# Performance work log

Measured on AMD Instinct MI355X. Metric: run time of the kernel, lower is better.

Reference implementation:

```python
import jax, jax.numpy as jnp
import numpy as np

EPS = float(np.finfo(np.float32).eps)
SEQ_LEN = 2048
NUM_HEADS = 16
DIM_EMB = 1024
DIM_HEAD = DIM_EMB // NUM_HEADS
DIM_K = DIM_EMB  # module scales by full dim_k, not per-head dim
BATCH = 2


def cosine_positional_encoding(seq_len, dim):
    idx = jnp.arange(seq_len, dtype=jnp.float32)
    scale = 1.0 / (10000.0 ** (jnp.arange(0, dim, 2, dtype=jnp.float32) / dim) + EPS)
    ang = idx[:, None] * scale[None, :]  # [S, dim/2]
    # interleave sin (even) and cos (odd) along last dim -> [S, dim]
    return jnp.stack([jnp.sin(ang), jnp.cos(ang)], axis=-1).reshape(seq_len, dim)


def setup_inputs() -> dict:
    key = jax.random.key(0)
    ks = jax.random.split(key, 5)
    s = DIM_EMB ** -0.5
    return {
        "x": jax.random.normal(ks[0], (BATCH, SEQ_LEN, DIM_EMB), dtype=jnp.float32),
        "Wq": jax.random.normal(ks[1], (DIM_EMB, DIM_EMB), dtype=jnp.float32) * s,
        "Wk": jax.random.normal(ks[2], (DIM_EMB, DIM_EMB), dtype=jnp.float32) * s,
        "Wv": jax.random.normal(ks[3], (DIM_EMB, DIM_EMB), dtype=jnp.float32) * s,
        "Wo": jax.random.normal(ks[4], (DIM_EMB, DIM_EMB), dtype=jnp.float32) * s,
    }


def reference(x, Wq, Wk, Wv, Wo):
    B, S, E = x.shape
    pos = cosine_positional_encoding(S, DIM_HEAD)  # [S, dim_head]
    # projections (bias-free)
    def split_heads(t):
        return t.reshape(B, S, NUM_HEADS, DIM_HEAD).transpose(0, 2, 1, 3)  # [B,H,S,D]
    q = split_heads(x @ Wq) + pos[None, None]
    k = split_heads(x @ Wk) + pos[None, None]
    v = split_heads(x @ Wv)
    scores = jnp.einsum("bhqd,bhkd->bhqk", q, k) * (DIM_K ** -0.5)
    causal_mask = jnp.triu(jnp.ones((S, S), dtype=bool), k=1)
    m_inf = -jnp.finfo(scores.dtype).max
    scores = jnp.where(causal_mask[None, None], m_inf, scores)
    attn = jax.nn.softmax(scores, axis=-1)
    out = jnp.einsum("bhqk,bhkd->bhqd", attn, v)
    out = out.transpose(0, 2, 1, 3).reshape(B, S, E)
    return out @ Wo
```

## Files before the change

kernel.cpp:

```cpp
#include <hip/hip_runtime.h>
#include <math.h>

#define BATCH 2
#define SEQ   2048
#define EMB   1024
#define NHEAD 16
#define DHEAD 64
#define MROWS (BATCH*SEQ)
#define QKS   2048

typedef unsigned int  uint;
typedef unsigned short ushort;
typedef __attribute__((ext_vector_type(8))) short short8;
typedef __attribute__((ext_vector_type(4))) float f32x4;

__device__ __forceinline__ float exp2_fast(float x) {
    return __builtin_amdgcn_exp2f(x);
}

__global__ void pos_init(float* __restrict__ pos) {
    int s = blockIdx.x;
    int d = threadIdx.x;
    int i = d >> 1;
    float expo  = (float)(2 * i) / (float)DHEAD;
    float scale = 1.0f / (powf(10000.0f, expo) + 1.1920928955078125e-07f);
    float ang   = (float)s * scale;
    pos[s * DHEAD + d] = (d & 1) ? cosf(ang) : sinf(ang);
}

__device__ __forceinline__ uint pack_bf16x2(float a, float b) {
    union { float f; uint u; } x, y;
    x.f = a; y.f = b;
    uint ua = x.u + 0x7fffu + ((x.u >> 16) & 1u);
    uint ub = y.u + 0x7fffu + ((y.u >> 16) & 1u);
    return (ua >> 16) | (ub & 0xffff0000u);
}
__device__ __forceinline__ ushort bf16_1(float a) {
    union { float f; uint u; } x; x.f = a;
    return (ushort)((x.u + 0x7fffu + ((x.u >> 16) & 1u)) >> 16);
}
__device__ __forceinline__ uint cvt_pk_bf16(float lo, float hi) {
    uint r;
    asm("v_cvt_pk_bf16_f32 %0, %1, %2" : "=v"(r) : "v"(lo), "v"(hi));
    return r;
}

__device__ __forceinline__ void gll16(const ushort* g, ushort* l) {
    __builtin_amdgcn_global_load_lds(
        (const __attribute__((address_space(1))) uint*)g,
        (__attribute__((address_space(3))) uint*)l, 16, 0, 0);
}

__global__ __launch_bounds__(256) void cvt_bf16(
    const float* __restrict__ in, ushort* __restrict__ out, int n2) {
    int gid = blockIdx.x * 256 + threadIdx.x;
    if (gid < n2) {
        float2 v = ((const float2*)in)[gid];
        ((uint*)out)[gid] = pack_bf16x2(v.x, v.y);
    }
}

__global__ __launch_bounds__(256) void wt_bf16_all(
    const float* __restrict__ Wq, const float* __restrict__ Wk,
    const float* __restrict__ Wv, const float* __restrict__ Wo,
    ushort* __restrict__ Wqkvt, ushort* __restrict__ Wot) {
    __shared__ float tile[32][33];
    const int which = blockIdx.z;
    const float* W = (which == 0) ? Wq : (which == 1) ? Wk : (which == 2) ? Wv : Wo;
    ushort* Wt = (which < 3) ? (Wqkvt + (size_t)which * 1024 * EMB) : Wot;
    const int c0 = blockIdx.x * 32;
    const int r0 = blockIdx.y * 32;
    const int tx = threadIdx.x & 31;
    const int ty = threadIdx.x >> 5;
#pragma unroll
    for (int i = 0; i < 4; ++i)
        tile[ty + i * 8][tx] = W[(size_t)(r0 + ty + i * 8) * EMB + c0 + tx];
    __syncthreads();
#pragma unroll
    for (int i = 0; i < 4; ++i)
        Wt[(size_t)(c0 + ty + i * 8) * EMB + r0 + tx] = bf16_1(tile[tx][ty + i * 8]);
}

#define TK 32
#define SCLQ (0.03125f * 1.44269504088896f)

template<int TMT>
__global__ __launch_bounds__(256) void gemm_mfma_t(
    const ushort* __restrict__ A, const ushort* __restrict__ Bt,
    void* __restrict__ Cv, ushort* __restrict__ VtOut,
    const float* __restrict__ pos, int posmode, int N, int K) {
    constexpr int MI = TMT / 32;
    __shared__ ushort As[TMT * TK];
    __shared__ ushort Bs[128 * TK];

    const int t    = threadIdx.x;
    const int lane = t & 63, w = t >> 6;
    const int quad = lane >> 4, l15 = lane & 15;
    const int bm = blockIdx.x * TMT, bn = blockIdx.y * 128;
    const int wm = (w & 1) * (TMT / 2), wn = (w >> 1) * 64;
    const int r0 = t >> 2, kp = (t & 3) * 8;

    f32x4 acc[MI][4];
#pragma unroll
    for (int mi = 0; mi < MI; ++mi)
#pragma unroll
        for (int ni = 0; ni < 4; ++ni)
            acc[mi][ni] = (f32x4){0.f, 0.f, 0.f, 0.f};

    for (int k0 = 0; k0 < K; k0 += TK) {
        __syncthreads();
#pragma unroll
        for (int i = 0; i < TMT / 64; ++i)
            gll16(A + (size_t)(bm + i * 64 + r0) * K + k0 + kp, &As[i * 2048 + t * 8]);
#pragma unroll
        for (int i = 0; i < 2; ++i)
            gll16(Bt + (size_t)(bn + i * 64 + r0) * K + k0 + kp, &Bs[i * 2048 + t * 8]);
        __syncthreads();

        short8 af[MI], bfv[4];
#pragma unroll
        for (int mi = 0; mi < MI; ++mi)
            af[mi] = *(const short8*)&As[(wm + mi * 16 + l15) * TK + quad * 8];
#pragma unroll
        for (int ni = 0; ni < 4; ++ni)
            bfv[ni] = *(const short8*)&Bs[(wn + ni * 16 + l15) * TK + quad * 8];
#pragma unroll
        for (int mi = 0; mi < MI; ++mi)
#pragma unroll
            for (int ni = 0; ni < 4; ++ni)
                acc[mi][ni] = __builtin_amdgcn_mfma_f32_16x16x32_bf16(
                    af[mi], bfv[ni], acc[mi][ni], 0, 0, 0);
    }

#pragma unroll
    for (int mi = 0; mi < MI; ++mi) {
        const int row0 = bm + wm + mi * 16 + quad * 4;
#pragma unroll
        for (int ni = 0; ni < 4; ++ni) {
            const int col = bn + wn + ni * 16 + l15;
            if (!posmode) {
#pragma unroll
                for (int r = 0; r < 4; ++r)
                    ((float*)Cv)[(size_t)(row0 + r) * N + col] = acc[mi][ni][r];
            } else if (col < 2048) {
#pragma unroll
                for (int r = 0; r < 4; ++r) {
                    const int row = row0 + r;
                    const int s   = row & (SEQ - 1);
                    float v = acc[mi][ni][r] + pos[s * DHEAD + (col & 63)];
                    if (col < 1024) v *= SCLQ;
                    ((ushort*)Cv)[(size_t)row * QKS + col] = bf16_1(v);
                }
            } else {
                const int hh = (col >> 6) & 15;
                const int d  = col & 63;
                const int bb = row0 >> 11;
                const int s0 = row0 & (SEQ - 1);
                uint2 u;
                u.x = pack_bf16x2(acc[mi][ni][0], acc[mi][ni][1]);
                u.y = pack_bf16x2(acc[mi][ni][2], acc[mi][ni][3]);
                *(uint2*)&VtOut[((size_t)(bb * 16 + hh) * 64 + d) * SEQ + s0] = u;
            }
        }
    }
}

#define LDP 72

__global__ __launch_bounds__(256) void attn_mfma8(
    const ushort* __restrict__ QK, const ushort* __restrict__ Vt,
    ushort* __restrict__ AOb) {
    __shared__ ushort Ks[64 * LDP];
    __shared__ ushort Vs[64 * LDP];
    __shared__ ushort Ps[64 * LDP];

    const int bid  = blockIdx.x;
    const int bh   = (bid & 7) + ((bid >> 8) << 3);
    const int qt   = 31 - ((bid >> 3) & 31);
    const int b    = bh >> 4, hd = bh & 15;
    const int t    = threadIdx.x;
    const int lane = t & 63, w = t >> 6;
    const int quad = lane >> 4, l15 = lane & 15;
    const int wrow = w * 16;
    const int sr = t >> 2;
    const int sc = (t & 3) * 16;

    const size_t qkbase = (size_t)b * SEQ * QKS + hd * 64;
    const ushort* kpb = QK + qkbase + 1024 + (size_t)sr * QKS + sc;
    const ushort* vpb = Vt + ((size_t)bh * 64 + sr) * SEQ;

    const ushort* qp = QK + qkbase + (size_t)(qt * 64 + wrow + l15) * QKS + quad * 8;
    const short8 aq0 = *(const short8*)qp;
    const short8 aq1 = *(const short8*)(qp + 32);

    uint4 ka = *(const uint4*)kpb;
    uint4 kb = *(const uint4*)(kpb + 8);
    uint4 va = *(const uint4*)(vpb + sc);
    uint4 vb = *(const uint4*)(vpb + sc + 8);

    f32x4 acc_o[4];
#pragma unroll
    for (int nd = 0; nd < 4; ++nd) acc_o[nd] = (f32x4){0.f, 0.f, 0.f, 0.f};
    float m_l = -3.0e38f, l_l = 0.f;
    const int qrow_g = qt * 64 + wrow + l15;

    for (int kt = 0; kt <= qt; ++kt) {
        __syncthreads();
        *(uint4*)&Ks[sr * LDP + sc]     = ka;
        *(uint4*)&Ks[sr * LDP + sc + 8] = kb;
        *(uint4*)&Vs[sr * LDP + sc]     = va;
        *(uint4*)&Vs[sr * LDP + sc + 8] = vb;
        const int ktn = (kt < qt) ? kt + 1 : qt;
        ka = *(const uint4*)(kpb + (size_t)ktn * 64 * QKS);
        kb = *(const uint4*)(kpb + (size_t)ktn * 64 * QKS + 8);
        va = *(const uint4*)(vpb + ktn * 64 + sc);
        vb = *(const uint4*)(vpb + ktn * 64 + sc + 8);
        __syncthreads();

        float sv[4][4];
        float pmax = -3.0e38f;
        const bool diag = (kt == qt);
        __builtin_amdgcn_s_setprio(1);
#pragma unroll
        for (int kg = 0; kg < 4; ++kg) {
            const short8 ak0 = *(const short8*)&Ks[(kg * 16 + l15) * LDP + quad * 8];
            const short8 ak1 = *(const short8*)&Ks[(kg * 16 + l15) * LDP + 32 + quad * 8];
            f32x4 a = (f32x4){0.f, 0.f, 0.f, 0.f};
            a = __builtin_amdgcn_mfma_f32_16x16x32_bf16(ak0, aq0, a, 0, 0, 0);
            a = __builtin_amdgcn_mfma_f32_16x16x32_bf16(ak1, aq1, a, 0, 0, 0);
            const int keyb = kt * 64 + kg * 16 + quad * 4;
#pragma unroll
            for (int r = 0; r < 4; ++r) {
                float v = a[r];
                if (diag && (keyb + r > qrow_g)) v = -3.0e38f;
                sv[kg][r] = v;
                pmax = fmaxf(pmax, v);
            }
        }
        __builtin_amdgcn_s_setprio(0);
        pmax = fmaxf(pmax, __shfl_xor(pmax, 16, 64));
        pmax = fmaxf(pmax, __shfl_xor(pmax, 32, 64));

        if (__any(pmax - m_l > 8.f)) {
            const float m_new = fmaxf(m_l, pmax);
            const float alpha = exp2_fast(m_l - m_new);
            m_l = m_new;
            l_l *= alpha;
            float av[4];
#pragma unroll
            for (int r = 0; r < 4; ++r) av[r] = __shfl(alpha, quad * 4 + r, 64);
#pragma unroll
            for (int nd = 0; nd < 4; ++nd)
#pragma unroll
                for (int r = 0; r < 4; ++r) acc_o[nd][r] *= av[r];
        }

        float rs = 0.f;
#pragma unroll
        for (int kg = 0; kg < 4; ++kg)
#pragma unroll
            for (int r = 0; r < 4; ++r) {
                float p = exp2_fast(sv[kg][r] - m_l);
                sv[kg][r] = p;
                rs += p;
            }
        rs += __shfl_xor(rs, 16, 64);
        rs += __shfl_xor(rs, 32, 64);
        l_l += rs;

        ushort* Pw = &Ps[wrow * LDP];
#pragma unroll
        for (int kg = 0; kg < 4; ++kg) {
            uint2 u;
            u.x = cvt_pk_bf16(sv[kg][0], sv[kg][1]);
            u.y = cvt_pk_bf16(sv[kg][2], sv[kg][3]);
            *(uint2*)&Pw[l15 * LDP + kg * 16 + quad * 4] = u;
        }
        const short8 pa0 = *(const short8*)&Pw[l15 * LDP + quad * 8];
        const short8 pa1 = *(const short8*)&Pw[l15 * LDP + 32 + quad * 8];
        __builtin_amdgcn_s_setprio(1);
#pragma unroll
        for (int nd = 0; nd < 4; ++nd) {
            const short8 bv0 = *(const short8*)&Vs[(nd * 16 + l15) * LDP + quad * 8];
            const short8 bv1 = *(const short8*)&Vs[(nd * 16 + l15) * LDP + 32 + quad * 8];
            acc_o[nd] = __builtin_amdgcn_mfma_f32_16x16x32_bf16(pa0, bv0, acc_o[nd], 0, 0, 0);
            acc_o[nd] = __builtin_amdgcn_mfma_f32_16x16x32_bf16(pa1, bv1, acc_o[nd], 0, 0, 0);
        }
        __builtin_amdgcn_s_setprio(0);
    }

    float linv[4];
#pragma unroll
    for (int r = 0; r < 4; ++r) linv[r] = 1.0f / __shfl(l_l, quad * 4 + r, 64);
#pragma unroll
    for (int nd = 0; nd < 4; ++nd)
#pragma unroll
        for (int r = 0; r < 4; ++r) {
            const int row = qt * 64 + wrow + quad * 4 + r;
            AOb[(size_t)(b * SEQ + row) * EMB + hd * 64 + nd * 16 + l15] =
                bf16_1(acc_o[nd][r] * linv[r]);
        }
}

#define BM 64
#define BN 64
#define BK 16

__global__ __launch_bounds__(256) void gemm_f32(
    const float* __restrict__ A, const float* __restrict__ B,
    float* __restrict__ C, const float* __restrict__ pos, int addpos,
    int M, int N, int K) {
    __shared__ float As[BK][BM];
    __shared__ float Bs[BK][BN];
    const int tid = threadIdx.x;
    const int bm  = blockIdx.x * BM;
    const int bn  = blockIdx.y * BN;
    const int tx  = tid & 15;
    const int ty  = tid >> 4;
    const int arow = tid >> 2;
    const int acol = (tid & 3) << 2;
    const int brow = tid >> 4;
    const int bcol = (tid & 15) << 2;
    float acc[4][4] = {{0.f}};
    const float* Aptr = A + (size_t)(bm + arow) * K + acol;
    const float* Bptr = B + (size_t)brow * N + bn + bcol;
    for (int k0 = 0; k0 < K; k0 += BK) {
        float4 av = *(const float4*)(Aptr + k0);
        float4 bv = *(const float4*)(Bptr + (size_t)k0 * N);
        __syncthreads();
        As[acol + 0][arow] = av.x;
        As[acol + 1][arow] = av.y;
        As[acol + 2][arow] = av.z;
        As[acol + 3][arow] = av.w;
        *(float4*)&Bs[brow][bcol] = bv;
        __syncthreads();
#pragma unroll
        for (int kk = 0; kk < BK; ++kk) {
            float4 a = *(const float4*)&As[kk][ty << 2];
            float4 b = *(const float4*)&Bs[kk][tx << 2];
            float aa[4] = {a.x, a.y, a.z, a.w};
            float bb[4] = {b.x, b.y, b.z, b.w};
#pragma unroll
            for (int i = 0; i < 4; ++i)
#pragma unroll
                for (int j = 0; j < 4; ++j)
                    acc[i][j] += aa[i] * bb[j];
        }
    }
#pragma unroll
    for (int i = 0; i < 4; ++i) {
        int m = bm + (ty << 2) + i;
        int n = bn + (tx << 2);
        float4 v = make_float4(acc[i][0], acc[i][1], acc[i][2], acc[i][3]);
        if (addpos) {
            int s = m & (SEQ - 1);
            int d = n & (DHEAD - 1);
            float4 p = *(const float4*)&pos[s * DHEAD + d];
            v.x += p.x; v.y += p.y; v.z += p.z; v.w += p.w;
        }
        *(float4*)&C[(size_t)m * N + n] = v;
    }
}

#define QT 128
#define KT 32
__global__ __launch_bounds__(QT) void attn_fwd(
    const float* __restrict__ Q, const float* __restrict__ Kg,
    const float* __restrict__ V, float* __restrict__ O) {
    __shared__ float Ks[KT][DHEAD];
    __shared__ float Vs[KT][DHEAD];
    const int t    = threadIdx.x;
    const int q0   = blockIdx.x * QT;
    const int bh   = blockIdx.y;
    const int b    = bh >> 4;
    const int h    = bh & 15;
    const int qrow = q0 + t;
    const size_t base = (size_t)b * SEQ * EMB + (size_t)h * DHEAD;
    float4 q4[16], o4[16];
#pragma unroll
    for (int i = 0; i < 16; ++i) {
        q4[i] = *(const float4*)&Q[base + (size_t)qrow * EMB + i * 4];
        o4[i] = make_float4(0.f, 0.f, 0.f, 0.f);
    }
    float m_i = -3.0e38f, l_i = 0.0f;
    const float scale = 0.03125f;
    const int kend = q0 + QT;
    for (int k0 = 0; k0 < kend; k0 += KT) {
        __syncthreads();
#pragma unroll
        for (int i = 0; i < 4; ++i) {
            int idx = t + i * QT;
            int r = idx >> 4;
            int c = (idx & 15) << 2;
            *(float4*)&Ks[r][c] = *(const float4*)&Kg[base + (size_t)(k0 + r) * EMB + c];
            *(float4*)&Vs[r][c] = *(const float4*)&V [base + (size_t)(k0 + r) * EMB + c];
        }
        __syncthreads();
        float sv[KT];
        float mt = m_i;
#pragma unroll
        for (int j = 0; j < KT; ++j) {
            const float4* kr = (const float4*)Ks[j];
            float dot = 0.f;
#pragma unroll
            for (int dd = 0; dd < 16; ++dd) {
                float4 kv = kr[dd];
                dot += q4[dd].x * kv.x + q4[dd].y * kv.y +
                       q4[dd].z * kv.z + q4[dd].w * kv.w;
            }
            sv[j] = (k0 + j <= qrow) ? dot * scale : -3.0e38f;
            mt = fmaxf(mt, sv[j]);
        }
        float corr = __expf(m_i - mt);
        l_i *= corr;
#pragma unroll
        for (int i = 0; i < 16; ++i) {
            o4[i].x *= corr; o4[i].y *= corr; o4[i].z *= corr; o4[i].w *= corr;
        }
#pragma unroll
        for (int j = 0; j < KT; ++j) {
            float pp = __expf(sv[j] - mt);
            l_i += pp;
            const float4* vr = (const float4*)Vs[j];
#pragma unroll
            for (int dd = 0; dd < 16; ++dd) {
                float4 vv = vr[dd];
                o4[dd].x += pp * vv.x; o4[dd].y += pp * vv.y;
                o4[dd].z += pp * vv.z; o4[dd].w += pp * vv.w;
            }
        }
        m_i = mt;
    }
    float inv = 1.0f / l_i;
#pragma unroll
    for (int i = 0; i < 16; ++i) {
        float4 v = o4[i];
        v.x *= inv; v.y *= inv; v.z *= inv; v.w *= inv;
        *(float4*)&O[base + (size_t)qrow * EMB + i * 4] = v;
    }
}

extern "C" void kernel_launch(void* const* d_in, const int* in_sizes, int n_in,
                              void* d_out, int out_size, void* d_ws, size_t ws_size,
                              hipStream_t stream) {
    const float* x  = (const float*)d_in[0];
    const float* Wq = (const float*)d_in[1];
    const float* Wk = (const float*)d_in[2];
    const float* Wv = (const float*)d_in[3];
    const float* Wo = (const float*)d_in[4];
    float* out = (float*)d_out;

    char* ws = (char*)d_ws;
    size_t off = 0;
    float*  pos   = (float*)(ws + off);  off += (size_t)SEQ * DHEAD * 4;
    ushort* xb    = (ushort*)(ws + off); off += (size_t)MROWS * EMB * 2;
    ushort* Wqkvt = (ushort*)(ws + off); off += (size_t)3072 * EMB * 2;
    ushort* Wot   = (ushort*)(ws + off); off += (size_t)EMB * EMB * 2;
    ushort* QKb   = (ushort*)(ws + off); off += (size_t)MROWS * QKS * 2;
    ushort* Vtp   = (ushort*)(ws + off); off += (size_t)MROWS * EMB * 2;
    ushort* AOb   = (ushort*)(ws + off); off += (size_t)MROWS * EMB * 2;
    const bool use_bf16 = off <= ws_size;

    const int M = MROWS, K = EMB;

    pos_init<<<SEQ, DHEAD, 0, stream>>>(pos);

    if (use_bf16) {
        const int n2 = MROWS * EMB / 2;
        cvt_bf16<<<n2 / 256, 256, 0, stream>>>(x, xb, n2);
        wt_bf16_all<<<dim3(EMB / 32, EMB / 32, 4), 256, 0, stream>>>(
            Wq, Wk, Wv, Wo, Wqkvt, Wot);

        gemm_mfma_t<128><<<dim3(M / 128, 3072 / 128), 256, 0, stream>>>(
            xb, Wqkvt, QKb, Vtp, pos, 1, 3072, K);

        attn_mfma8<<<dim3(1024), 256, 0, stream>>>(QKb, Vtp, AOb);

        gemm_mfma_t<64><<<dim3(M / 64, EMB / 128), 256, 0, stream>>>(
            AOb, Wot, out, nullptr, pos, 0, EMB, K);
    } else {
        size_t f = 0;
        float* posf = (float*)(ws + f); f += (size_t)SEQ * DHEAD * 4;
        float* Qb = (float*)(ws + f); f += (size_t)MROWS * EMB * 4;
        float* Kb = (float*)(ws + f); f += (size_t)MROWS * EMB * 4;
        float* Vb = (float*)(ws + f); f += (size_t)MROWS * EMB * 4;
        float* AO = (float*)(ws + f);
        dim3 g(M / BM, EMB / BN);
        gemm_f32<<<g, 256, 0, stream>>>(x, Wq, Qb, posf, 1, M, EMB, K);
        gemm_f32<<<g, 256, 0, stream>>>(x, Wk, Kb, posf, 1, M, EMB, K);
        gemm_f32<<<g, 256, 0, stream>>>(x, Wv, Vb, posf, 0, M, EMB, K);
        attn_fwd<<<dim3(SEQ / QT, BATCH * NHEAD), QT, 0, stream>>>(Qb, Kb, Vb, AO);
        gemm_f32<<<g, 256, 0, stream>>>(AO, Wo, out, posf, 0, M, EMB, K);
    }
}
```

Measured before the change: 213.4 us.

## Pair causal query tiles per block and double-buffer K/V in LDS

Each attention block now processes two query tiles (qt and 31-qt) so every block does a balanced amount of causal work, halving the grid to 512 blocks. K/V shared tiles are double-buffered, dropping one barrier per iteration. The inline-asm bf16 pack is replaced with the software rounding pack and s_setprio hints are removed. Fewer blocks may reduce occupancy or latency hiding on 256 CUs, and the software pack adds ALU work.

```diff
diff --git a/kernel.cpp b/kernel.cpp
--- a/kernel.cpp
+++ b/kernel.cpp
@@ -38,11 +38,6 @@
 __device__ __forceinline__ ushort bf16_1(float a) {
     union { float f; uint u; } x; x.f = a;
     return (ushort)((x.u + 0x7fffu + ((x.u >> 16) & 1u)) >> 16);
-}
-__device__ __forceinline__ uint cvt_pk_bf16(float lo, float hi) {
-    uint r;
-    asm("v_cvt_pk_bf16_f32 %0, %1, %2" : "=v"(r) : "v"(lo), "v"(hi));
-    return r;
 }
 
 __device__ __forceinline__ void gll16(const ushort* g, ushort* l) {
@@ -167,16 +162,16 @@
 
 #define LDP 72
 
-__global__ __launch_bounds__(256) void attn_mfma8(
+__global__ __launch_bounds__(256) void attn_mfma9(
     const ushort* __restrict__ QK, const ushort* __restrict__ Vt,
     ushort* __restrict__ AOb) {
-    __shared__ ushort Ks[64 * LDP];
-    __shared__ ushort Vs[64 * LDP];
+    __shared__ ushort Ks[2][64 * LDP];
+    __shared__ ushort Vs[2][64 * LDP];
     __shared__ ushort Ps[64 * LDP];
 
     const int bid  = blockIdx.x;
-    const int bh   = (bid & 7) + ((bid >> 8) << 3);
-    const int qt   = 31 - ((bid >> 3) & 31);
+    const int bh   = (bid & 7) | (((bid >> 7) & 3) << 3);
+    const int pair = (bid >> 3) & 15;
     const int b    = bh >> 4, hd = bh & 15;
     const int t    = threadIdx.x;
     const int lane = t & 63, w = t >> 6;
@@ -189,117 +184,121 @@
     const ushort* kpb = QK + qkbase + 1024 + (size_t)sr * QKS + sc;
     const ushort* vpb = Vt + ((size_t)bh * 64 + sr) * SEQ;
 
-    const ushort* qp = QK + qkbase + (size_t)(qt * 64 + wrow + l15) * QKS + quad * 8;
-    const short8 aq0 = *(const short8*)qp;
-    const short8 aq1 = *(const short8*)(qp + 32);
-
     uint4 ka = *(const uint4*)kpb;
     uint4 kb = *(const uint4*)(kpb + 8);
     uint4 va = *(const uint4*)(vpb + sc);
     uint4 vb = *(const uint4*)(vpb + sc + 8);
-
-    f32x4 acc_o[4];
-#pragma unroll
-    for (int nd = 0; nd < 4; ++nd) acc_o[nd] = (f32x4){0.f, 0.f, 0.f, 0.f};
-    float m_l = -3.0e38f, l_l = 0.f;
-    const int qrow_g = qt * 64 + wrow + l15;
-
-    for (int kt = 0; kt <= qt; ++kt) {
-        __syncthreads();
-        *(uint4*)&Ks[sr * LDP + sc]     = ka;
-        *(uint4*)&Ks[sr * LDP + sc + 8] = kb;
-        *(uint4*)&Vs[sr * LDP + sc]     = va;
-        *(uint4*)&Vs[sr * LDP + sc + 8] = vb;
-        const int ktn = (kt < qt) ? kt + 1 : qt;
-        ka = *(const uint4*)(kpb + (size_t)ktn * 64 * QKS);
-        kb = *(const uint4*)(kpb + (size_t)ktn * 64 * QKS + 8);
-        va = *(const uint4*)(vpb + ktn * 64 + sc);
-        vb = *(const uint4*)(vpb + ktn * 64 + sc + 8);
-        __syncthreads();
-
-        float sv[4][4];
-        float pmax = -3.0e38f;
-        const bool diag = (kt == qt);
-        __builtin_amdgcn_s_setprio(1);
-#pragma unroll
-        for (int kg = 0; kg < 4; ++kg) {
-            const short8 ak0 = *(const short8*)&Ks[(kg * 16 + l15) * LDP + quad * 8];
-            const short8 ak1 = *(const short8*)&Ks[(kg * 16 + l15) * LDP + 32 + quad * 8];
-            f32x4 a = (f32x4){0.f, 0.f, 0.f, 0.f};
-            a = __builtin_amdgcn_mfma_f32_16x16x32_bf16(ak0, aq0, a, 0, 0, 0);
-            a = __builtin_amdgcn_mfma_f32_16x16x32_bf16(ak1, aq1, a, 0, 0, 0);
-            const int keyb = kt * 64 + kg * 16 + quad * 4;
+    int cur = 0;
+
+#pragma unroll
+    for (int ph = 0; ph < 2; ++ph) {
+        const int qt = ph ? (31 - pair) : pair;
+
+        const ushort* qp = QK + qkbase + (size_t)(qt * 64 + wrow + l15) * QKS + quad * 8;
+        const short8 aq0 = *(const short8*)qp;
+        const short8 aq1 = *(const short8*)(qp + 32);
+
+        f32x4 acc_o[4];
+#pragma unroll
+        for (int nd = 0; nd < 4; ++nd) acc_o[nd] = (f32x4){0.f, 0.f, 0.f, 0.f};
+        float m_l = -3.0e38f, l_l = 0.f;
+        const int qrow_g = qt * 64 + wrow + l15;
+
+        for (int kt = 0; kt <= qt; ++kt) {
+            ushort* Kc = Ks[cur];
+            ushort* Vc = Vs[cur];
+            *(uint4*)&Kc[sr * LDP + sc]     = ka;
+            *(uint4*)&Kc[sr * LDP + sc + 8] = kb;
+            *(uint4*)&Vc[sr * LDP + sc]     = va;
+            *(uint4*)&Vc[sr * LDP + sc + 8] = vb;
+            const int ktn = (kt < qt) ? kt + 1 : 0;
+            ka = *(const uint4*)(kpb + (size_t)ktn * 64 * QKS);
+            kb = *(const uint4*)(kpb + (size_t)ktn * 64 * QKS + 8);
+            va = *(const uint4*)(vpb + ktn * 64 + sc);
+            vb = *(const uint4*)(vpb + ktn * 64 + sc + 8);
+            __syncthreads();
+
+            float sv[4][4];
+            float pmax = -3.0e38f;
+            const bool diag = (kt == qt);
+#pragma unroll
+            for (int kg = 0; kg < 4; ++kg) {
+                const short8 ak0 = *(const short8*)&Kc[(kg * 16 + l15) * LDP + quad * 8];
+                const short8 ak1 = *(const short8*)&Kc[(kg * 16 + l15) * LDP + 32 + quad * 8];
+                f32x4 a = (f32x4){0.f, 0.f, 0.f, 0.f};
+                a = __builtin_amdgcn_mfma_f32_16x16x32_bf16(ak0, aq0, a, 0, 0, 0);
+                a = __builtin_amdgcn_mfma_f32_16x16x32_bf16(ak1, aq1, a, 0, 0, 0);
+                const int keyb = kt * 64 + kg * 16 + quad * 4;
+#pragma unroll
+                for (int r = 0; r < 4; ++r) {
+                    float v = a[r];
+                    if (diag && (keyb + r > qrow_g)) v = -3.0e38f;
+                    sv[kg][r] = v;
+                    pmax = fmaxf(pmax, v);
+                }
+            }
+            pmax = fmaxf(pmax, __shfl_xor(pmax, 16, 64));
+            pmax = fmaxf(pmax, __shfl_xor(pmax, 32, 64));
+
+            if (__any(pmax - m_l > 8.f)) {
+                const float m_new = fmaxf(m_l, pmax);
+                const float alpha = exp2_fast(m_l - m_new);
+                m_l = m_new;
+                l_l *= alpha;
+                float av[4];
+#pragma unroll
+                for (int r = 0; r < 4; ++r) av[r] = __shfl(alpha, quad * 4 + r, 64);
+#pragma unroll
+                for (int nd = 0; nd < 4; ++nd)
+#pragma unroll
+                    for (int r = 0; r < 4; ++r) acc_o[nd][r] *= av[r];
+            }
+
+            float rs = 0.f;
+#pragma unroll
+            for (int kg = 0; kg < 4; ++kg)
+#pragma unroll
+                for (int r = 0; r < 4; ++r) {
+                    float p = exp2_fast(sv[kg][r] - m_l);
+                    sv[kg][r] = p;
+                    rs += p;
+                }
+            rs += __shfl_xor(rs, 16, 64);
+            rs += __shfl_xor(rs, 32, 64);
+            l_l += rs;
+
+            ushort* Pw = &Ps[wrow * LDP];
+#pragma unroll
+            for (int kg = 0; kg < 4; ++kg) {
+                uint2 u;
+                u.x = pack_bf16x2(sv[kg][0], sv[kg][1]);
+                u.y = pack_bf16x2(sv[kg][2], sv[kg][3]);
+                *(uint2*)&Pw[l15 * LDP + kg * 16 + quad * 4] = u;
+            }
+            const short8 pa0 = *(const short8*)&Pw[l15 * LDP + quad * 8];
+            const short8 pa1 = *(const short8*)&Pw[l15 * LDP + 32 + quad * 8];
+#pragma unroll
+            for (int nd = 0; nd < 4; ++nd) {
+                const short8 bv0 = *(const short8*)&Vc[(nd * 16 + l15) * LDP + quad * 8];
+                const short8 bv1 = *(const short8*)&Vc[(nd * 16 + l15) * LDP + 32 + quad * 8];
+                acc_o[nd] = __builtin_amdgcn_mfma_f32_16x16x32_bf16(pa0, bv0, acc_o[nd], 0, 0, 0);
+                acc_o[nd] = __builtin_amdgcn_mfma_f32_16x16x32_bf16(pa1, bv1, acc_o[nd], 0, 0, 0);
+            }
+            cur ^= 1;
+        }
+
+        float linv[4];
+#pragma unroll
+        for (int r = 0; r < 4; ++r) linv[r] = 1.0f / __shfl(l_l, quad * 4 + r, 64);
+#pragma unroll
+        for (int nd = 0; nd < 4; ++nd)
 #pragma unroll
             for (int r = 0; r < 4; ++r) {
-                float v = a[r];
-                if (diag && (keyb + r > qrow_g)) v = -3.0e38f;
-                sv[kg][r] = v;
-                pmax = fmaxf(pmax, v);
-            }
-        }
-        __builtin_amdgcn_s_setprio(0);
-        pmax = fmaxf(pmax, __shfl_xor(pmax, 16, 64));
-        pmax = fmaxf(pmax, __shfl_xor(pmax, 32, 64));
-
-        if (__any(pmax - m_l > 8.f)) {
-            const float m_new = fmaxf(m_l, pmax);
-            const float alpha = exp2_fast(m_l - m_new);
-            m_l = m_new;
-            l_l *= alpha;
-            float av[4];
-#pragma unroll
-            for (int r = 0; r < 4; ++r) av[r] = __shfl(alpha, quad * 4 + r, 64);
-#pragma unroll
-            for (int nd = 0; nd < 4; ++nd)
-#pragma unroll
-                for (int r = 0; r < 4; ++r) acc_o[nd][r] *= av[r];
-        }
-
-        float rs = 0.f;
-#pragma unroll
-        for (int kg = 0; kg < 4; ++kg)
-#pragma unroll
-            for (int r = 0; r < 4; ++r) {
-                float p = exp2_fast(sv[kg][r] - m_l);
-                sv[kg][r] = p;
-                rs += p;
-            }
-        rs += __shfl_xor(rs, 16, 64);
-        rs += __shfl_xor(rs, 32, 64);
-        l_l += rs;
-
-        ushort* Pw = &Ps[wrow * LDP];
-#pragma unroll
-        for (int kg = 0; kg < 4; ++kg) {
-            uint2 u;
-            u.x = cvt_pk_bf16(sv[kg][0], sv[kg][1]);
-            u.y = cvt_pk_bf16(sv[kg][2], sv[kg][3]);
-            *(uint2*)&Pw[l15 * LDP + kg * 16 + quad * 4] = u;
-        }
-        const short8 pa0 = *(const short8*)&Pw[l15 * LDP + quad * 8];
-        const short8 pa1 = *(const short8*)&Pw[l15 * LDP + 32 + quad * 8];
-        __builtin_amdgcn_s_setprio(1);
-#pragma unroll
-        for (int nd = 0; nd < 4; ++nd) {
-            const short8 bv0 = *(const short8*)&Vs[(nd * 16 + l15) * LDP + quad * 8];
-            const short8 bv1 = *(const short8*)&Vs[(nd * 16 + l15) * LDP + 32 + quad * 8];
-            acc_o[nd] = __builtin_amdgcn_mfma_f32_16x16x32_bf16(pa0, bv0, acc_o[nd], 0, 0, 0);
-            acc_o[nd] = __builtin_amdgcn_mfma_f32_16x16x32_bf16(pa1, bv1, acc_o[nd], 0, 0, 0);
-        }
-        __builtin_amdgcn_s_setprio(0);
-    }
-
-    float linv[4];
-#pragma unroll
-    for (int r = 0; r < 4; ++r) linv[r] = 1.0f / __shfl(l_l, quad * 4 + r, 64);
-#pragma unroll
-    for (int nd = 0; nd < 4; ++nd)
-#pragma unroll
-        for (int r = 0; r < 4; ++r) {
-            const int row = qt * 64 + wrow + quad * 4 + r;
-            AOb[(size_t)(b * SEQ + row) * EMB + hd * 64 + nd * 16 + l15] =
-                bf16_1(acc_o[nd][r] * linv[r]);
-        }
+                const int row = qt * 64 + wrow + quad * 4 + r;
+                AOb[(size_t)(b * SEQ + row) * EMB + hd * 64 + nd * 16 + l15] =
+                    bf16_1(acc_o[nd][r] * linv[r]);
+            }
+    }
 }
 
 #define BM 64
@@ -474,7 +473,7 @@
         gemm_mfma_t<128><<<dim3(M / 128, 3072 / 128), 256, 0, stream>>>(
             xb, Wqkvt, QKb, Vtp, pos, 1, 3072, K);
 
-        attn_mfma8<<<dim3(1024), 256, 0, stream>>>(QKb, Vtp, AOb);
+        attn_mfma9<<<dim3(512), 256, 0, stream>>>(QKb, Vtp, AOb);
 
         gemm_mfma_t<64><<<dim3(M / 64, EMB / 128), 256, 0, stream>>>(
             AOb, Wot, out, nullptr, pos, 0, EMB, K);
```

Result: faster. 195.4 us (-8.5%).
